# Kernel tuning notes

Hardware: AMD Instinct MI355X
Metric: run time of the kernel (lower is better)

The kernel has to match this reference:

```python
import jax, jax.numpy as jnp
import numpy as np

N = 50000   # nodes
E = 500000  # edges
D = 128     # enc_dim == Hout
INIT_W = 0.1


def _lin_w(k, din, dout):
    return jax.random.normal(k, (dout, din), jnp.float32) * INIT_W


def setup_inputs() -> dict:
    key = jax.random.key(0)
    ks = jax.random.split(key, 16)
    inp = {
        "x": jax.random.normal(ks[0], (N, D), jnp.float32),
        "src": jax.random.randint(ks[1], (E,), 0, N),
        "dst": jax.random.randint(ks[2], (E,), 0, N),
        # encoders (Linear enc_dim -> enc_dim)
        "WencK": _lin_w(ks[3], D, D), "bencK": jnp.zeros((D,), jnp.float32),
        "WencP1": _lin_w(ks[4], D, D), "bencP1": jnp.zeros((D,), jnp.float32),
        "WencP2": _lin_w(ks[5], D, D), "bencP2": jnp.zeros((D,), jnp.float32),
        # Kfun: Linear-Tanh-Linear-ReLU-Linear
        "K0W": _lin_w(ks[6], D, D), "K0b": jnp.zeros((D,), jnp.float32),
        "K1W": _lin_w(ks[7], D, D), "K1b": jnp.zeros((D,), jnp.float32),
        "K2W": _lin_w(ks[8], D, D), "K2b": jnp.zeros((D,), jnp.float32),
        # Ufun: Linear-Tanh-Linear-ReLU-Linear
        "U0W": _lin_w(ks[9], D, D), "U0b": jnp.zeros((D,), jnp.float32),
        "U1W": _lin_w(ks[10], D, D), "U1b": jnp.zeros((D,), jnp.float32),
        "U2W": _lin_w(ks[11], D, D), "U2b": jnp.zeros((D,), jnp.float32),
    }
    return inp


def _mlp3(h, W0, b0, W1, b1, W2, b2):
    h = jnp.tanh(h @ W0.T + b0)
    h = jax.nn.relu(h @ W1.T + b1)
    return h @ W2.T + b2


def reference(x, src, dst,
              WencK, bencK, WencP1, bencP1, WencP2, bencP2,
              K0W, K0b, K1W, K1b, K2W, K2b,
              U0W, U0b, U1W, U1b, U2W, U2b):
    # getK: encode nodes, copy_u + sum to dst, node MLP
    h1 = x @ WencK.T + bencK                                   # [N, D]
    h1_agg = jax.ops.segment_sum(h1[src], dst, num_segments=N)  # [N, D]
    Knode = _mlp3(h1_agg, K0W, K0b, K1W, K1b, K2W, K2b)         # [N, D]
    # getU: u_add_v on encoded features, edge MLP
    p1 = x @ WencP1.T + bencP1
    p2 = x @ WencP2.T + bencP2
    Eedge = _mlp3(p1[src] + p2[dst], U0W, U0b, U1W, U1b, U2W, U2b)  # [E, D]
    # getH: u_mul_e + sum to dst
    Enew = jax.ops.segment_sum(Knode[src] * Eedge, dst, num_segments=N)  # [N, D]
    return jnp.sum(Enew)
```

## Files before the change

kernel.cpp:

```cpp
#include <hip/hip_runtime.h>
#include <hip/hip_bf16.h>
#include <math.h>

#define NN 50000
#define NE 500000
#define DD 128
#define STR 136
#define NSCAN (2 * NN)
#define SCAN_BLK ((NSCAN + 1023) / 1024)
#define HIST_BLK ((NE + 255) / 256)
#define CVT_BLK  ((NN * DD + 4095) / 4096)
#define PRECONV_BLK ((7 * 2048 + 1023) / 1024)
#define ENC_BLK  ((NN + 127) / 128)

typedef __attribute__((ext_vector_type(8))) short short8;
typedef __attribute__((ext_vector_type(4))) float floatx4;

__device__ __forceinline__ float bf2f(unsigned short u) {
    unsigned v = ((unsigned)u) << 16;
    float f;
    __builtin_memcpy(&f, &v, 4);
    return f;
}
__device__ __forceinline__ unsigned short f2bf(float f) {
    unsigned x;
    __builtin_memcpy(&x, &f, 4);
    x += 0x7FFF + ((x >> 16) & 1);
    return (unsigned short)(x >> 16);
}
__device__ __forceinline__ float fast_tanh(float x) {
    float t = __builtin_amdgcn_exp2f(x * 2.88539008177793f);
    return 1.f - 2.f * __builtin_amdgcn_rcpf(t + 1.f);
}

__global__ __launch_bounds__(256) void k1_kernel(
    const int* __restrict__ src, const int* __restrict__ dst,
    int* __restrict__ cnt_dst, int* __restrict__ cnt_src,
    int* __restrict__ rank_d, int* __restrict__ rank_s,
    const float* __restrict__ x, unsigned short* __restrict__ xbf,
    const float* __restrict__ U0W, const float* __restrict__ WencP1,
    const float* __restrict__ WencP2, const float* __restrict__ K0W,
    const float* __restrict__ WencK,
    const float* __restrict__ bp1, const float* __restrict__ bp2,
    const float* __restrict__ U0b, const float* __restrict__ bk,
    const float* __restrict__ U2b,
    float* __restrict__ comp, float* __restrict__ bvecs)
{
    __shared__ float Bs[DD * DD];
    int blk = blockIdx.x;
    int t = threadIdx.x;

    if (blk < HIST_BLK) {
        int e = blk * 256 + t;
        if (e < NE) {
            rank_d[e] = atomicAdd(&cnt_dst[dst[e]], 1);
            rank_s[e] = atomicAdd(&cnt_src[src[e]], 1);
        }
        return;
    }
    if (blk < HIST_BLK + CVT_BLK) {
        int base = (blk - HIST_BLK) * 4096;
        #pragma unroll
        for (int j = 0; j < 4; ++j) {
            int idx = base + (j * 256 + t) * 4;
            if (idx < NN * DD) {
                float4 f = *(const float4*)&x[idx];
                ushort4 v4;
                v4.x = f2bf(f.x); v4.y = f2bf(f.y);
                v4.z = f2bf(f.z); v4.w = f2bf(f.w);
                *(ushort4*)&xbf[idx] = v4;
            }
        }
        return;
    }

    int b = blk - (HIST_BLK + CVT_BLK);
    if (b == 6) {
        if (t < 128) {
            float s1 = 0.f, s2 = 0.f;
            for (int k = 0; k < DD; ++k) {
                s1 += U0W[t * DD + k] * (bp1[k] + bp2[k]);
                s2 += K0W[t * DD + k] * bk[k];
            }
            bvecs[t] = s1 + U0b[t];
            bvecs[128 + t] = s2;
            int f = (t & 64) + 16 * (t & 3) + ((t & 63) >> 2);
            bvecs[256 + t] = U2b[f];
        }
        return;
    }
    int mat = b >> 1, half = b & 1;
    const float* A = (mat == 2) ? K0W : U0W;
    const float* B = (mat == 0) ? WencP1 : (mat == 1) ? WencP2 : WencK;
    float* C = comp + (size_t)mat * DD * DD;
    for (int i = 0; i < 64; ++i)
        Bs[i * 256 + t] = B[i * 256 + t];
    __syncthreads();
    int row = half * 64 + (t >> 2);
    int j0 = (t & 3) * 32;
    float acc[32];
    #pragma unroll
    for (int jj = 0; jj < 32; ++jj) acc[jj] = 0.f;
    for (int k = 0; k < DD; ++k) {
        float a = A[row * DD + k];
        #pragma unroll
        for (int jj = 0; jj < 32; ++jj)
            acc[jj] += a * Bs[k * DD + j0 + jj];
    }
    #pragma unroll
    for (int jj = 0; jj < 32; ++jj) C[row * DD + j0 + jj] = acc[jj];
}

__global__ __launch_bounds__(1024) void k2_kernel(
    const float* __restrict__ comp, const float* __restrict__ K1W,
    const float* __restrict__ K2W, const float* __restrict__ U2W,
    const float* __restrict__ U1W, unsigned short* __restrict__ wfrag,
    const int* __restrict__ cnt, int* __restrict__ base, int* __restrict__ bsum)
{
    int t = threadIdx.x;
    if (blockIdx.x < PRECONV_BLK) {
        int g = blockIdx.x * 1024 + t;
        if (g >= 7 * 2048) return;
        int m = g >> 11;
        int rem = g & 2047;
        int kt = rem >> 9, nt = (rem >> 6) & 7, lane = rem & 63;
        const float* W;
        bool perm = false, tr = false;
        switch (m) {
            case 0: W = comp; break;
            case 1: W = comp + 16384; break;
            case 2: W = comp + 32768; break;
            case 3: W = K1W; perm = true; break;
            case 4: W = K2W; perm = true; break;
            case 5: W = U2W; perm = true; tr = true; break;
            default: W = U1W; break;
        }
        int n = nt * 16 + (lane & 15);
        #pragma unroll
        for (int j = 0; j < 8; ++j) {
            int ks = kt * 32 + (lane >> 4) * 8 + j;
            int f = perm ? (ks & 64) + 16 * (ks & 3) + ((ks & 63) >> 2) : ks;
            float v = tr ? W[f * DD + n] : W[n * DD + f];
            wfrag[(size_t)g * 8 + j] = f2bf(v);
        }
        return;
    }
    __shared__ int wsum[16];
    int sb = blockIdx.x - PRECONV_BLK;
    int i = sb * 1024 + t;
    int v = (i < NSCAN) ? cnt[i] : 0;
    int lane = t & 63, w = t >> 6;
    int xv = v;
    #pragma unroll
    for (int off = 1; off < 64; off <<= 1) {
        int y = __shfl_up(xv, off);
        if (lane >= off) xv += y;
    }
    if (lane == 63) wsum[w] = xv;
    __syncthreads();
    if (w == 0) {
        int s = (lane < 16) ? wsum[lane] : 0;
        #pragma unroll
        for (int off = 1; off < 16; off <<= 1) {
            int y = __shfl_up(s, off);
            if (lane >= off) s += y;
        }
        if (lane < 16) wsum[lane] = s;
    }
    __syncthreads();
    int wavebase = (w == 0) ? 0 : wsum[w - 1];
    int incl = wavebase + xv;
    if (i < NSCAN) base[i] = incl - v;
    if (t == 1023) bsum[sb] = incl;
}

__global__ __launch_bounds__(128) void scan2_kernel(
    int* __restrict__ bsum, float* __restrict__ out)
{
    if (threadIdx.x == 0 && blockIdx.x == 0) *out = 0.f;
    __shared__ int wsum[2];
    int t = threadIdx.x;
    int v = (t < SCAN_BLK) ? bsum[t] : 0;
    int lane = t & 63, w = t >> 6;
    int x = v;
    #pragma unroll
    for (int off = 1; off < 64; off <<= 1) {
        int y = __shfl_up(x, off);
        if (lane >= off) x += y;
    }
    if (lane == 63) wsum[w] = x;
    __syncthreads();
    int wavebase = (w == 0) ? 0 : wsum[0];
    int incl = wavebase + x;
    if (t < SCAN_BLK) bsum[t] = incl - v;
}

__global__ __launch_bounds__(256) void place_kernel(
    const int* __restrict__ src, const int* __restrict__ dst,
    const int* __restrict__ base, const int* __restrict__ bsum,
    const int* __restrict__ rank_d, const int* __restrict__ rank_s,
    int* __restrict__ sorted_src_bydst, int2* __restrict__ epairs)
{
    int e = blockIdx.x * 256 + threadIdx.x;
    if (e < NE) {
        int s = src[e], d = dst[e];
        sorted_src_bydst[base[d] + bsum[d >> 10] + rank_d[e]] = s;
        int si = NN + s;
        int p = base[si] + bsum[si >> 10] + rank_s[e] - NE;
        epairs[p] = make_int2(s, d);
    }
}

__global__ __launch_bounds__(256) void agg_kernel(
    const unsigned short* __restrict__ xbf,
    const int* __restrict__ base, const int* __restrict__ bsum,
    const int* __restrict__ cnt, const int* __restrict__ sorted_src,
    unsigned short* __restrict__ xagg)
{
    int node = blockIdx.x * 4 + (threadIdx.x >> 6);
    int lane = threadIdx.x & 63;
    if (node >= NN) return;
    int lo = base[node] + bsum[node >> 10];
    int hi = lo + cnt[node];
    float ax = 0.f, ay = 0.f;
    for (int off = lo; off < hi; off += 64) {
        int myid = (off + lane < hi) ? sorted_src[off + lane] : 0;
        int nk = min(64, hi - off);
        int k = 0;
        for (; k + 4 <= nk; k += 4) {
            int s0 = __shfl(myid, k);
            int s1 = __shfl(myid, k + 1);
            int s2 = __shfl(myid, k + 2);
            int s3 = __shfl(myid, k + 3);
            ushort2 v0 = *(const ushort2*)&xbf[(size_t)s0 * DD + lane * 2];
            ushort2 v1 = *(const ushort2*)&xbf[(size_t)s1 * DD + lane * 2];
            ushort2 v2 = *(const ushort2*)&xbf[(size_t)s2 * DD + lane * 2];
            ushort2 v3 = *(const ushort2*)&xbf[(size_t)s3 * DD + lane * 2];
            ax += bf2f(v0.x) + bf2f(v1.x) + bf2f(v2.x) + bf2f(v3.x);
            ay += bf2f(v0.y) + bf2f(v1.y) + bf2f(v2.y) + bf2f(v3.y);
        }
        for (; k < nk; ++k) {
            int s = __shfl(myid, k);
            ushort2 v = *(const ushort2*)&xbf[(size_t)s * DD + lane * 2];
            ax += bf2f(v.x);
            ay += bf2f(v.y);
        }
    }
    ushort2 o;
    o.x = f2bf(ax); o.y = f2bf(ay);
    *(ushort2*)&xagg[(size_t)node * DD + lane * 2] = o;
}

__global__ __launch_bounds__(256) void encnode_kernel(
    const float* __restrict__ x, const unsigned short* __restrict__ xagg,
    const unsigned short* __restrict__ wf, const float* __restrict__ bvecs,
    const int* __restrict__ cnt,
    const float* __restrict__ K0b, const float* __restrict__ K1b,
    const float* __restrict__ K2b,
    unsigned short* __restrict__ q1, unsigned short* __restrict__ q2,
    unsigned short* __restrict__ Km, float* __restrict__ kb)
{
    __shared__ unsigned short A[128 * STR];
    const int t = threadIdx.x;
    const int lane = t & 63, w = t >> 6;
    const int wm = w >> 1, wn = w & 1;
    const int c = lane & 15, q = lane >> 4;

    if (blockIdx.x < ENC_BLK) {
        const int row0 = blockIdx.x * 128;
        #pragma unroll
        for (int i = 0; i < 16; ++i) {
            int idx = i * 256 + t;
            int r = idx >> 5, ch = idx & 31;
            int gr = row0 + r;
            ushort4 v4 = {0, 0, 0, 0};
            if (gr < NN) {
                float4 f = *(const float4*)&x[(size_t)gr * DD + ch * 4];
                v4.x = f2bf(f.x); v4.y = f2bf(f.y);
                v4.z = f2bf(f.z); v4.w = f2bf(f.w);
            }
            *(ushort4*)&A[r * STR + ch * 4] = v4;
        }
        __syncthreads();

        for (int l = 0; l < 2; ++l) {
            floatx4 acc[4][4];
            #pragma unroll
            for (int i = 0; i < 4; ++i)
                #pragma unroll
                for (int j = 0; j < 4; ++j)
                    acc[i][j] = (floatx4){0.f, 0.f, 0.f, 0.f};
            const short8* W8 = (const short8*)(wf + (size_t)l * 16384);
            #pragma unroll
            for (int kt = 0; kt < 4; ++kt) {
                short8 af[4], bfr[4];
                #pragma unroll
                for (int i = 0; i < 4; ++i)
                    af[i] = *(const short8*)&A[(wm * 64 + i * 16 + c) * STR + kt * 32 + q * 8];
                #pragma unroll
                for (int j = 0; j < 4; ++j)
                    bfr[j] = W8[(kt * 8 + wn * 4 + j) * 64 + lane];
                #pragma unroll
                for (int i = 0; i < 4; ++i)
                    #pragma unroll
                    for (int j = 0; j < 4; ++j)
                        acc[i][j] = __builtin_amdgcn_mfma_f32_16x16x32_bf16(af[i], bfr[j], acc[i][j], 0, 0, 0);
            }
            unsigned short* pp = (l == 0) ? q1 : q2;
            float bv[4];
            #pragma unroll
            for (int j = 0; j < 4; ++j)
                bv[j] = (l == 0) ? bvecs[c + 16 * j + 64 * wn] : 0.f;

            #pragma unroll
            for (int i = 0; i < 4; ++i)
                #pragma unroll
                for (int r = 0; r < 4; ++r) {
                    int node = row0 + wm * 64 + i * 16 + 4 * q + r;
                    if (node < NN) {
                        #pragma unroll
                        for (int j = 0; j < 4; ++j)
                            pp[(size_t)node * DD + c + 16 * j + 64 * wn] = f2bf(acc[i][j][r] + bv[j]);
                    }
                }
        }
        return;
    }

    const int row0 = (blockIdx.x - ENC_BLK) * 128;
    #pragma unroll
    for (int i = 0; i < 8; ++i) {
        int idx = i * 256 + t;
        int r = idx >> 4, ch = idx & 15;
        int gr = row0 + r;
        short8 v = (short8){0,0,0,0,0,0,0,0};
        if (gr < NN) v = *(const short8*)&xagg[(size_t)gr * DD + ch * 8];
        *(short8*)&A[r * STR + ch * 8] = v;
    }
    __syncthreads();

    for (int l = 0; l < 4; ++l) {
        floatx4 acc[4][4];
        #pragma unroll
        for (int i = 0; i < 4; ++i)
            #pragma unroll
            for (int j = 0; j < 4; ++j)
                acc[i][j] = (floatx4){0.f, 0.f, 0.f, 0.f};
        const short8* W8 = (const short8*)(wf + (size_t)(2 + l) * 16384);
        #pragma unroll
        for (int kt = 0; kt < 4; ++kt) {
            short8 af[4], bfr[4];
            #pragma unroll
            for (int i = 0; i < 4; ++i)
                af[i] = *(const short8*)&A[(wm * 64 + i * 16 + c) * STR + kt * 32 + q * 8];
            #pragma unroll
            for (int j = 0; j < 4; ++j)
                bfr[j] = W8[(kt * 8 + wn * 4 + j) * 64 + lane];
            #pragma unroll
            for (int i = 0; i < 4; ++i)
                #pragma unroll
                for (int j = 0; j < 4; ++j)
                    acc[i][j] = __builtin_amdgcn_mfma_f32_16x16x32_bf16(af[i], bfr[j], acc[i][j], 0, 0, 0);
        }

        if (l < 3) {
            const float* bb = (l == 0) ? K0b : (l == 1) ? K1b : K2b;
            float bv[4];
            #pragma unroll
            for (int j = 0; j < 4; ++j) bv[j] = bb[c + 16 * j + 64 * wn];
            float bvv[4];
            #pragma unroll
            for (int j = 0; j < 4; ++j)
                bvv[j] = (l == 0) ? bvecs[128 + c + 16 * j + 64 * wn] : 0.f;

            __syncthreads();
            #pragma unroll
            for (int i = 0; i < 4; ++i)
                #pragma unroll
                for (int r = 0; r < 4; ++r) {
                    int node = row0 + wm * 64 + i * 16 + 4 * q + r;
                    float cn = (l == 0) ? (float)((node < NN) ? cnt[node] : 0) : 0.f;
                    float v0 = acc[i][0][r] + bv[0] + cn * bvv[0];
                    float v1 = acc[i][1][r] + bv[1] + cn * bvv[1];
                    float v2 = acc[i][2][r] + bv[2] + cn * bvv[2];
                    float v3 = acc[i][3][r] + bv[3] + cn * bvv[3];
                    if (l == 0) {
                        v0 = fast_tanh(v0); v1 = fast_tanh(v1);
                        v2 = fast_tanh(v2); v3 = fast_tanh(v3);
                    } else if (l == 1) {
                        v0 = fmaxf(v0, 0.f); v1 = fmaxf(v1, 0.f);
                        v2 = fmaxf(v2, 0.f); v3 = fmaxf(v3, 0.f);
                    }
                    ushort4 pk;
                    pk.x = f2bf(v0); pk.y = f2bf(v1); pk.z = f2bf(v2); pk.w = f2bf(v3);
                    int m = wm * 64 + i * 16 + 4 * q + r;
                    *(ushort4*)&A[m * STR + 4 * c + 64 * wn] = pk;
                }
            __syncthreads();

            if (l == 2) {
                if (t < 128) {
                    int node = row0 + t;
                    if (node < NN) {
                        float s = 0.f;
                        #pragma unroll
                        for (int ch = 0; ch < 16; ++ch) {
                            short8 v = *(const short8*)&A[t * STR + ch * 8];
                            #pragma unroll
                            for (int e = 0; e < 8; ++e)
                                s += bf2f((unsigned short)v[e]) * bvecs[256 + ch * 8 + e];
                        }
                        kb[node] = s;
                    }
                }
            }
        } else {
            #pragma unroll
            for (int i = 0; i < 4; ++i)
                #pragma unroll
                for (int r = 0; r < 4; ++r) {
                    int node = row0 + wm * 64 + i * 16 + 4 * q + r;
                    if (node < NN) {
                        ushort4 pk;
                        pk.x = f2bf(acc[i][0][r]);
                        pk.y = f2bf(acc[i][1][r]);
                        pk.z = f2bf(acc[i][2][r]);
                        pk.w = f2bf(acc[i][3][r]);
                        *(ushort4*)&Km[(size_t)node * DD + 4 * c + 64 * wn] = pk;
                    }
                }
        }
    }
}

__global__ __launch_bounds__(256) void edge_kernel(
    const unsigned short* __restrict__ q1, const unsigned short* __restrict__ q2,
    const unsigned short* __restrict__ Km, const float* __restrict__ kb,
    const int2* __restrict__ epairs,
    const unsigned short* __restrict__ wf, const float* __restrict__ U1b,
    float* __restrict__ out)
{
    __shared__ unsigned short A[128 * STR];
    __shared__ int sidx[128];
    __shared__ int didx[128];
    __shared__ float red[4];
    const int t = threadIdx.x;
    const int lane = t & 63, w = t >> 6;
    const int wm = w >> 1, wn = w & 1;
    const int c = lane & 15, q = lane >> 4;
    const int e0 = blockIdx.x * 128;

    if (t < 128) {
        int e = e0 + t;
        if (e < NE) {
            int2 p = epairs[e];
            sidx[t] = p.x;
            didx[t] = p.y;
        } else {
            sidx[t] = -1;
            didx[t] = 0;
        }
    }
    __syncthreads();

    float part = 0.f;
    if (t < 128 && sidx[t] >= 0) part += kb[sidx[t]];

    #pragma unroll
    for (int i = 0; i < 8; ++i) {
        int idx = i * 256 + t;
        int r = idx >> 4, ch = idx & 15;
        int s = sidx[r];
        int o32[4] = {0, 0, 0, 0};
        if (s >= 0) {
            short8 a8 = *(const short8*)&q1[(size_t)s * DD + ch * 8];
            short8 b8 = *(const short8*)&q2[(size_t)didx[r] * DD + ch * 8];
            #pragma unroll
            for (int k = 0; k < 8; k += 2) {
                float2 u;
                u.x = fast_tanh(bf2f((unsigned short)a8[k])     + bf2f((unsigned short)b8[k]));
                u.y = fast_tanh(bf2f((unsigned short)a8[k + 1]) + bf2f((unsigned short)b8[k + 1]));
                __hip_bfloat162 hb = __float22bfloat162_rn(u);
                __builtin_memcpy(&o32[k >> 1], &hb, 4);
            }
        }
        *(int4*)&A[r * STR + ch * 8] = *(int4*)o32;
    }
    __syncthreads();

    floatx4 acc[4][4];
    #pragma unroll
    for (int i = 0; i < 4; ++i)
        #pragma unroll
        for (int j = 0; j < 4; ++j)
            acc[i][j] = (floatx4){0.f, 0.f, 0.f, 0.f};
    const short8* W8 = (const short8*)(wf + (size_t)6 * 16384);
    #pragma unroll
    for (int kt = 0; kt < 4; ++kt) {
        short8 af[4], bfr[4];
        #pragma unroll
        for (int i = 0; i < 4; ++i)
            af[i] = *(const short8*)&A[(wm * 64 + i * 16 + c) * STR + kt * 32 + q * 8];
        #pragma unroll
        for (int j = 0; j < 4; ++j)
            bfr[j] = W8[(kt * 8 + wn * 4 + j) * 64 + lane];
        #pragma unroll
        for (int i = 0; i < 4; ++i)
            #pragma unroll
            for (int j = 0; j < 4; ++j)
                acc[i][j] = __builtin_amdgcn_mfma_f32_16x16x32_bf16(af[i], bfr[j], acc[i][j], 0, 0, 0);
    }
    float bv[4];
    #pragma unroll
    for (int j = 0; j < 4; ++j) bv[j] = U1b[c + 16 * j + 64 * wn];

    #pragma unroll
    for (int i = 0; i < 4; ++i)
        #pragma unroll
        for (int r = 0; r < 4; ++r) {
            int m = wm * 64 + i * 16 + 4 * q + r;
            int s = sidx[m];
            if (s >= 0) {
                ushort4 km4 = *(const ushort4*)&Km[(size_t)s * DD + 4 * c + 64 * wn];
                part += fmaxf(acc[i][0][r] + bv[0], 0.f) * bf2f(km4.x)
                      + fmaxf(acc[i][1][r] + bv[1], 0.f) * bf2f(km4.y)
                      + fmaxf(acc[i][2][r] + bv[2], 0.f) * bf2f(km4.z)
                      + fmaxf(acc[i][3][r] + bv[3], 0.f) * bf2f(km4.w);
            }
        }

    #pragma unroll
    for (int off = 32; off > 0; off >>= 1)
        part += __shfl_down(part, off);
    if (lane == 0) red[w] = part;
    __syncthreads();
    if (t == 0)
        atomicAdd(out, red[0] + red[1] + red[2] + red[3]);
}

extern "C" void kernel_launch(void* const* d_in, const int* in_sizes, int n_in,
                              void* d_out, int out_size, void* d_ws, size_t ws_size,
                              hipStream_t stream)
{
    const float* x     = (const float*)d_in[0];
    const int*   src   = (const int*)  d_in[1];
    const int*   dst   = (const int*)  d_in[2];
    const float* WencK = (const float*)d_in[3];
    const float* bencK = (const float*)d_in[4];
    const float* WencP1= (const float*)d_in[5];
    const float* bencP1= (const float*)d_in[6];
    const float* WencP2= (const float*)d_in[7];
    const float* bencP2= (const float*)d_in[8];
    const float* K0W   = (const float*)d_in[9];
    const float* K0b   = (const float*)d_in[10];
    const float* K1W   = (const float*)d_in[11];
    const float* K1b   = (const float*)d_in[12];
    const float* K2W   = (const float*)d_in[13];
    const float* K2b   = (const float*)d_in[14];
    const float* U0W   = (const float*)d_in[15];
    const float* U0b   = (const float*)d_in[16];
    const float* U1W   = (const float*)d_in[17];
    const float* U1b   = (const float*)d_in[18];
    const float* U2W   = (const float*)d_in[19];
    const float* U2b   = (const float*)d_in[20];

    char* ws = (char*)d_ws;
    unsigned short* wfrag = (unsigned short*)ws;
    float* comp  = (float*)(ws + 0x40000);
    float* bvecs = (float*)(ws + 0x70000);
    unsigned short* xbf  = (unsigned short*)(ws + 0x71000);
    unsigned short* q1   = xbf + (size_t)NN * DD;
    unsigned short* q2   = q1 + (size_t)NN * DD;
    unsigned short* Kmg  = q2 + (size_t)NN * DD;
    unsigned short* xagg = Kmg + (size_t)NN * DD;
    float* kb       = (float*)(xagg + (size_t)NN * DD);
    int* cnt_dst    = (int*)(kb + NN);
    int* cnt_src    = cnt_dst + NN;
    int* base       = cnt_src + NN;
    int* bsum       = base + NSCAN;
    int* rank_d     = bsum + 128;
    int* rank_s     = rank_d + NE;
    int* sorted_src_bydst = rank_s + NE;
    int2* epairs    = (int2*)(sorted_src_bydst + NE);

    hipMemsetAsync(cnt_dst, 0, 2 * NN * sizeof(int), stream);

    k1_kernel<<<HIST_BLK + CVT_BLK + 7, 256, 0, stream>>>(
        src, dst, cnt_dst, cnt_src, rank_d, rank_s, x, xbf,
        U0W, WencP1, WencP2, K0W, WencK, bencP1, bencP2, U0b, bencK, U2b,
        comp, bvecs);

    k2_kernel<<<PRECONV_BLK + SCAN_BLK, 1024, 0, stream>>>(
        comp, K1W, K2W, U2W, U1W, wfrag, cnt_dst, base, bsum);

    scan2_kernel<<<1, 128, 0, stream>>>(bsum, (float*)d_out);

    place_kernel<<<HIST_BLK, 256, 0, stream>>>(
        src, dst, base, bsum, rank_d, rank_s, sorted_src_bydst, epairs);

    agg_kernel<<<(NN + 3) / 4, 256, 0, stream>>>(
        xbf, base, bsum, cnt_dst, sorted_src_bydst, xagg);

    encnode_kernel<<<2 * ENC_BLK, 256, 0, stream>>>(
        x, xagg, wfrag, bvecs, cnt_dst, K0b, K1b, K2b, q1, q2, Kmg, kb);

    edge_kernel<<<(NE + 127) / 128, 256, 0, stream>>>(
        q1, q2, Kmg, kb, epairs, wfrag, U1b, (float*)d_out);
}
```

Baseline: 327.3 us.

## Widen agg gathers to 16B, prefold tanh scale into weights, batch q2 loads

The aggregation kernel now has each wave process 4 neighbors at once, with 16-byte short8 loads per lane instead of 4-byte ushort2, and reduces the partials across lane groups with shuffles. The tanh pre-scale constant is folded into the composed U0 weight matrices and bias, which removes a multiply per element in the edge kernel. The edge kernel also issues its q2 gathers in batches of four before the q1 loads and tanh, so more memory requests are in flight. The risks are higher register pressure, and a change in bf16 rounding because the scale is applied before quantization to bf16.

```diff
diff --git a/kernel.cpp b/kernel.cpp
--- a/kernel.cpp
+++ b/kernel.cpp
@@ -12,6 +12,7 @@
 #define CVT_BLK  ((NN * DD + 4095) / 4096)
 #define PRECONV_BLK ((7 * 2048 + 1023) / 1024)
 #define ENC_BLK  ((NN + 127) / 128)
+#define TSCALE 2.885390081777927f
 
 typedef __attribute__((ext_vector_type(8))) short short8;
 typedef __attribute__((ext_vector_type(4))) float floatx4;
@@ -29,7 +30,11 @@
     return (unsigned short)(x >> 16);
 }
 __device__ __forceinline__ float fast_tanh(float x) {
-    float t = __builtin_amdgcn_exp2f(x * 2.88539008177793f);
+    float t = __builtin_amdgcn_exp2f(x * TSCALE);
+    return 1.f - 2.f * __builtin_amdgcn_rcpf(t + 1.f);
+}
+__device__ __forceinline__ float fast_tanh_pre(float u) {
+    float t = __builtin_amdgcn_exp2f(u);
     return 1.f - 2.f * __builtin_amdgcn_rcpf(t + 1.f);
 }
 
@@ -82,7 +87,7 @@
                 s1 += U0W[t * DD + k] * (bp1[k] + bp2[k]);
                 s2 += K0W[t * DD + k] * bk[k];
             }
-            bvecs[t] = s1 + U0b[t];
+            bvecs[t] = (s1 + U0b[t]) * TSCALE;
             bvecs[128 + t] = s2;
             int f = (t & 64) + 16 * (t & 3) + ((t & 63) >> 2);
             bvecs[256 + t] = U2b[f];
@@ -92,6 +97,7 @@
     int mat = b >> 1, half = b & 1;
     const float* A = (mat == 2) ? K0W : U0W;
     const float* B = (mat == 0) ? WencP1 : (mat == 1) ? WencP2 : WencK;
+    float scl = (mat == 2) ? 1.f : TSCALE;
     float* C = comp + (size_t)mat * DD * DD;
     for (int i = 0; i < 64; ++i)
         Bs[i * 256 + t] = B[i * 256 + t];
@@ -108,7 +114,7 @@
             acc[jj] += a * Bs[k * DD + j0 + jj];
     }
     #pragma unroll
-    for (int jj = 0; jj < 32; ++jj) C[row * DD + j0 + jj] = acc[jj];
+    for (int jj = 0; jj < 32; ++jj) C[row * DD + j0 + jj] = acc[jj] * scl;
 }
 
 __global__ __launch_bounds__(1024) void k2_kernel(
@@ -222,33 +228,37 @@
     if (node >= NN) return;
     int lo = base[node] + bsum[node >> 10];
     int hi = lo + cnt[node];
-    float ax = 0.f, ay = 0.f;
+    const int rowg = lane >> 4;
+    const int colc = lane & 15;
+    float a[8];
+    #pragma unroll
+    for (int j = 0; j < 8; ++j) a[j] = 0.f;
+
     for (int off = lo; off < hi; off += 64) {
         int myid = (off + lane < hi) ? sorted_src[off + lane] : 0;
         int nk = min(64, hi - off);
-        int k = 0;
-        for (; k + 4 <= nk; k += 4) {
-            int s0 = __shfl(myid, k);
-            int s1 = __shfl(myid, k + 1);
-            int s2 = __shfl(myid, k + 2);
-            int s3 = __shfl(myid, k + 3);
-            ushort2 v0 = *(const ushort2*)&xbf[(size_t)s0 * DD + lane * 2];
-            ushort2 v1 = *(const ushort2*)&xbf[(size_t)s1 * DD + lane * 2];
-            ushort2 v2 = *(const ushort2*)&xbf[(size_t)s2 * DD + lane * 2];
-            ushort2 v3 = *(const ushort2*)&xbf[(size_t)s3 * DD + lane * 2];
-            ax += bf2f(v0.x) + bf2f(v1.x) + bf2f(v2.x) + bf2f(v3.x);
-            ay += bf2f(v0.y) + bf2f(v1.y) + bf2f(v2.y) + bf2f(v3.y);
-        }
-        for (; k < nk; ++k) {
-            int s = __shfl(myid, k);
-            ushort2 v = *(const ushort2*)&xbf[(size_t)s * DD + lane * 2];
-            ax += bf2f(v.x);
-            ay += bf2f(v.y);
-        }
-    }
-    ushort2 o;
-    o.x = f2bf(ax); o.y = f2bf(ay);
-    *(ushort2*)&xagg[(size_t)node * DD + lane * 2] = o;
+        for (int k = 0; k < nk; k += 4) {
+            int kk = k + rowg;
+            int s = __shfl(myid, kk);
+            if (kk < nk) {
+                short8 v = *(const short8*)&xbf[(size_t)s * DD + colc * 8];
+                #pragma unroll
+                for (int j = 0; j < 8; ++j)
+                    a[j] += bf2f((unsigned short)v[j]);
+            }
+        }
+    }
+    #pragma unroll
+    for (int j = 0; j < 8; ++j) {
+        a[j] += __shfl_xor(a[j], 16);
+        a[j] += __shfl_xor(a[j], 32);
+    }
+    if (lane < 16) {
+        short8 o;
+        #pragma unroll
+        for (int j = 0; j < 8; ++j) o[j] = (short)f2bf(a[j]);
+        *(short8*)&xagg[(size_t)node * DD + lane * 8] = o;
+    }
 }
 
 __global__ __launch_bounds__(256) void encnode_kernel(
@@ -467,24 +477,35 @@
     if (t < 128 && sidx[t] >= 0) part += kb[sidx[t]];
 
     #pragma unroll
-    for (int i = 0; i < 8; ++i) {
-        int idx = i * 256 + t;
-        int r = idx >> 4, ch = idx & 15;
-        int s = sidx[r];
-        int o32[4] = {0, 0, 0, 0};
-        if (s >= 0) {
-            short8 a8 = *(const short8*)&q1[(size_t)s * DD + ch * 8];
-            short8 b8 = *(const short8*)&q2[(size_t)didx[r] * DD + ch * 8];
-            #pragma unroll
-            for (int k = 0; k < 8; k += 2) {
-                float2 u;
-                u.x = fast_tanh(bf2f((unsigned short)a8[k])     + bf2f((unsigned short)b8[k]));
-                u.y = fast_tanh(bf2f((unsigned short)a8[k + 1]) + bf2f((unsigned short)b8[k + 1]));
-                __hip_bfloat162 hb = __float22bfloat162_rn(u);
-                __builtin_memcpy(&o32[k >> 1], &hb, 4);
-            }
-        }
-        *(int4*)&A[r * STR + ch * 8] = *(int4*)o32;
+    for (int half = 0; half < 2; ++half) {
+        short8 qbv[4];
+        int rr[4], cc[4], ss[4];
+        #pragma unroll
+        for (int i = 0; i < 4; ++i) {
+            int idx = (half * 4 + i) * 256 + t;
+            int r = idx >> 4, ch = idx & 15;
+            int s = sidx[r];
+            rr[i] = r; cc[i] = ch; ss[i] = s;
+            if (s >= 0)
+                qbv[i] = *(const short8*)&q2[(size_t)didx[r] * DD + ch * 8];
+        }
+        #pragma unroll
+        for (int i = 0; i < 4; ++i) {
+            int o32[4] = {0, 0, 0, 0};
+            if (ss[i] >= 0) {
+                short8 a8 = *(const short8*)&q1[(size_t)ss[i] * DD + cc[i] * 8];
+                short8 b8 = qbv[i];
+                #pragma unroll
+                for (int k = 0; k < 8; k += 2) {
+                    float2 u;
+                    u.x = fast_tanh_pre(bf2f((unsigned short)a8[k])     + bf2f((unsigned short)b8[k]));
+                    u.y = fast_tanh_pre(bf2f((unsigned short)a8[k + 1]) + bf2f((unsigned short)b8[k + 1]));
+                    __hip_bfloat162 hb = __float22bfloat162_rn(u);
+                    __builtin_memcpy(&o32[k >> 1], &hb, 4);
+                }
+            }
+            *(int4*)&A[rr[i] * STR + cc[i] * 8] = *(int4*)o32;
+        }
     }
     __syncthreads();
 
```

Measured after the change: 329.1 us. No clear change (+0.5%).
